# Kernel tuning notes

Hardware: AMD Instinct MI355X
Metric: run time of the kernel (lower is better)

## Reference

```python
import jax, jax.numpy as jnp
import numpy as np

LN_EPS = 1e-5


def setup_inputs() -> dict:
    N, E, D = 50000, 800000, 128
    H = 4 * D
    key = jax.random.key(0)
    ks = jax.random.split(key, 8)
    h = jax.random.normal(ks[0], (N, D), dtype=jnp.float32)
    e_ij = jax.random.normal(ks[1], (E, D), dtype=jnp.float32)
    src = jax.random.randint(ks[2], (E,), 0, N, dtype=jnp.int32)
    dst = jax.random.randint(ks[3], (E,), 0, N, dtype=jnp.int32)
    # MLP params (torch nn.Linear default-style scale)
    W1 = jax.random.normal(ks[4], (D, H), dtype=jnp.float32) / np.sqrt(D)
    b1 = jnp.zeros((H,), dtype=jnp.float32)
    W2 = jax.random.normal(ks[5], (H, D), dtype=jnp.float32) / np.sqrt(H)
    b2 = jnp.zeros((D,), dtype=jnp.float32)
    gamma = jnp.ones((D,), dtype=jnp.float32)
    beta = jnp.zeros((D,), dtype=jnp.float32)
    return {"h": h, "e_ij": e_ij, "src": src, "dst": dst,
            "W1": W1, "b1": b1, "W2": W2, "b2": b2,
            "gamma": gamma, "beta": beta}


def reference(h, e_ij, src, dst, W1, b1, W2, b2, gamma, beta):
    N = h.shape[0]
    # update_all(copy_u('h'), sum): sum source-node features at each destination
    neigh = jax.ops.segment_sum(h[src], dst, num_segments=N)
    # update_all(copy_edge('e_ij'), sum): sum edge features at each destination
    u_edge = jax.ops.segment_sum(e_ij, dst, num_segments=N)
    u = neigh + u_edge                      # [N, D]
    # MLP: D -> 4D -> D with ReLU, then residual
    hid = jax.nn.relu(u @ W1 + b1)          # [N, 4D]
    out = hid @ W2 + b2 + h                 # [N, D]
    # LayerNorm over feature dim
    mean = jnp.mean(out, axis=-1, keepdims=True)
    var = jnp.var(out, axis=-1, keepdims=True)
    normed = (out - mean) * jax.lax.rsqrt(var + LN_EPS)
    # dropout with training=False is identity
    return normed * gamma + beta
```

## Files before the change

kernel.cpp:

```cpp
#include <hip/hip_runtime.h>

#define BM 64

typedef __bf16 bf16x8 __attribute__((ext_vector_type(8)));
typedef float f32x4 __attribute__((ext_vector_type(4)));
typedef float f4 __attribute__((ext_vector_type(4)));

__device__ __forceinline__ unsigned short f2bf(float x) {
  unsigned int u = __builtin_bit_cast(unsigned int, x);
  u += 0x7fffu + ((u >> 16) & 1u);
  return (unsigned short)(u >> 16);
}

__device__ __forceinline__ int swz(int row, int col) {
  return (row * 128 + col) ^ ((row & 7) << 3);
}

__device__ __forceinline__ f4 ntload4(const float* p) {
  return __builtin_nontemporal_load((const f4*)p);
}

__device__ __forceinline__ int wave_incl_scan(int v, int lane) {
  #pragma unroll
  for (int off = 1; off < 64; off <<= 1) {
    int t = __shfl_up(v, off, 64);
    if (lane >= off) v += t;
  }
  return v;
}

__global__ __launch_bounds__(256) void prep_weights(
    const float* __restrict__ W1, const float* __restrict__ W2,
    unsigned short* __restrict__ W1T, unsigned short* __restrict__ W2T,
    int* __restrict__ counts, int N) {
  int t = blockIdx.x * 256 + threadIdx.x;
  if (t < N) counts[t] = 0;
  {
    int hh = t >> 7, kk = t & 127;
    W1T[t] = f2bf(W1[kk * 512 + hh]);
  }
  {
    int dd = t >> 9, hh = t & 511;
    W2T[t] = f2bf(W2[hh * 128 + dd]);
  }
}

__global__ __launch_bounds__(256) void hist_dst(const int* __restrict__ dst,
                                                int* counts, int E) {
  int i = blockIdx.x * 256 + threadIdx.x;
  if (i < E) atomicAdd(&counts[dst[i]], 1);
}

__global__ __launch_bounds__(256) void scan1(const int* __restrict__ counts,
                                             int* offs, int* btot, int N) {
  int i = blockIdx.x * 256 + threadIdx.x;
  int lane = threadIdx.x & 63, wv = threadIdx.x >> 6;
  int v = (i < N) ? counts[i] : 0;
  int incl = wave_incl_scan(v, lane);
  __shared__ int wt[4];
  if (lane == 63) wt[wv] = incl;
  __syncthreads();
  int wpre = 0;
  for (int w = 0; w < wv; ++w) wpre += wt[w];
  if (i < N) offs[i] = wpre + incl - v;
  if (threadIdx.x == 255) btot[blockIdx.x] = wpre + incl;
}

__global__ __launch_bounds__(64) void scan2(int* btot, int nb) {
  int lane = threadIdx.x;
  __shared__ int carry_s;
  if (lane == 0) carry_s = 0;
  __syncthreads();
  for (int base = 0; base < nb; base += 64) {
    int i = base + lane;
    int v = (i < nb) ? btot[i] : 0;
    int incl = wave_incl_scan(v, lane);
    int carry = carry_s;
    if (i < nb) btot[i] = carry + incl - v;
    __syncthreads();
    if (lane == 63) carry_s = carry + incl;
    __syncthreads();
  }
}

__global__ __launch_bounds__(256) void scan3(int* offs, const int* __restrict__ btot,
                                             int N) {
  int i = blockIdx.x * 256 + threadIdx.x;
  if (i < N) offs[i] += btot[blockIdx.x];
}

__global__ __launch_bounds__(256) void build_perm(const int* __restrict__ dst,
                                                  const int* __restrict__ src,
                                                  int* offs, int2* perm2, int E) {
  int i = blockIdx.x * 256 + threadIdx.x;
  if (i < E) {
    int p = atomicAdd(&offs[dst[i]], 1);
    perm2[p] = make_int2(i, src[i]);
  }
}

__global__ __launch_bounds__(256) void gather_sum(
    const float* __restrict__ hfeat, const float* __restrict__ eij,
    const int2* __restrict__ perm2,
    const int* __restrict__ offs, const int* __restrict__ counts,
    float* __restrict__ u, int N) {
  int node = blockIdx.x * 4 + (threadIdx.x >> 6);
  if (node >= N) return;
  int lane = threadIdx.x & 63;
  int half = lane >> 5, c4 = (lane & 31) * 4;
  int cnt = counts[node];
  int beg = offs[node] - cnt;
  f4 acc = (f4){0.f, 0.f, 0.f, 0.f};
  for (int base = 0; base < cnt; base += 64) {
    int m = cnt - base; if (m > 64) m = 64;
    int2 es = perm2[beg + base + (lane < m ? lane : m - 1)];
    int k = 0;
    for (; 2 * k + 8 <= m; k += 4) {
      int i0 = 2 * k + half;
      int e0 = __shfl(es.x, i0, 64),     s0 = __shfl(es.y, i0, 64);
      int e1 = __shfl(es.x, i0 + 2, 64), s1 = __shfl(es.y, i0 + 2, 64);
      int e2 = __shfl(es.x, i0 + 4, 64), s2 = __shfl(es.y, i0 + 4, 64);
      int e3 = __shfl(es.x, i0 + 6, 64), s3 = __shfl(es.y, i0 + 6, 64);
      f4 ev0 = ntload4(eij + (size_t)e0 * 128 + c4);
      f4 ev1 = ntload4(eij + (size_t)e1 * 128 + c4);
      f4 ev2 = ntload4(eij + (size_t)e2 * 128 + c4);
      f4 ev3 = ntload4(eij + (size_t)e3 * 128 + c4);
      f4 hv0 = *(const f4*)(hfeat + (size_t)s0 * 128 + c4);
      f4 hv1 = *(const f4*)(hfeat + (size_t)s1 * 128 + c4);
      f4 hv2 = *(const f4*)(hfeat + (size_t)s2 * 128 + c4);
      f4 hv3 = *(const f4*)(hfeat + (size_t)s3 * 128 + c4);
      acc += (ev0 + hv0) + (ev1 + hv1) + (ev2 + hv2) + (ev3 + hv3);
    }
    for (; 2 * k < m; ++k) {
      int idx = 2 * k + half;
      int e = __shfl(es.x, idx & 63, 64), s = __shfl(es.y, idx & 63, 64);
      if (idx < m) {
        f4 ev = ntload4(eij + (size_t)e * 128 + c4);
        f4 hv = *(const f4*)(hfeat + (size_t)s * 128 + c4);
        acc += ev + hv;
      }
    }
  }
  acc.x += __shfl_xor(acc.x, 32, 64);
  acc.y += __shfl_xor(acc.y, 32, 64);
  acc.z += __shfl_xor(acc.z, 32, 64);
  acc.w += __shfl_xor(acc.w, 32, 64);
  if (half == 0) *(f4*)(u + (size_t)node * 128 + c4) = acc;
}

__global__ __launch_bounds__(256, 2) void fused_mlp_ln(
    float* uo, const float* __restrict__ hfeat,
    const unsigned short* __restrict__ W1T, const unsigned short* __restrict__ W2T,
    const float* __restrict__ b1, const float* __restrict__ b2,
    const float* __restrict__ gma, const float* __restrict__ bta, int N) {
  __shared__ unsigned short As[BM * 128];
  __shared__ unsigned short Hs[BM * 128];
  __shared__ unsigned short Bs[128 * 128];

  const int tid = threadIdx.x;
  const int wave = tid >> 6, lane = tid & 63;
  const int lo = lane & 15, hi = lane >> 4;
  const int bm0 = blockIdx.x * BM;
  const int arow = wave * 16 + lo;

  #pragma unroll
  for (int i = 0; i < 8; ++i) {
    int q = i * 256 + tid;
    int r = q >> 5, c4 = (q & 31) * 4;
    f4 v = (f4){0.f, 0.f, 0.f, 0.f};
    if (bm0 + r < N) v = *(const f4*)(uo + (size_t)(bm0 + r) * 128 + c4);
    uint2 bv;
    bv.x = (unsigned)f2bf(v.x) | ((unsigned)f2bf(v.y) << 16);
    bv.y = (unsigned)f2bf(v.z) | ((unsigned)f2bf(v.w) << 16);
    *(uint2*)(&As[swz(r, c4)]) = bv;
  }

  f32x4 acc2[8];
  #pragma unroll
  for (int n = 0; n < 8; ++n) acc2[n] = (f32x4){0.f, 0.f, 0.f, 0.f};

  for (int c = 0; c < 4; ++c) {
    __syncthreads();
    #pragma unroll
    for (int i = 0; i < 8; ++i) {
      int q = i * 256 + tid;
      int r = q >> 4, c8 = (q & 15) * 8;
      uint4 w = *(const uint4*)(W1T + ((size_t)(c * 128 + r) * 128 + c8));
      *(uint4*)(&Bs[swz(r, c8)]) = w;
    }
    __syncthreads();

    f32x4 acc1[8];
    #pragma unroll
    for (int n = 0; n < 8; ++n) acc1[n] = (f32x4){0.f, 0.f, 0.f, 0.f};
    #pragma unroll
    for (int kk = 0; kk < 4; ++kk) {
      bf16x8 a = *(const bf16x8*)(&As[swz(arow, kk * 32 + hi * 8)]);
      #pragma unroll
      for (int n = 0; n < 8; ++n) {
        bf16x8 b = *(const bf16x8*)(&Bs[swz(n * 16 + lo, kk * 32 + hi * 8)]);
        acc1[n] = __builtin_amdgcn_mfma_f32_16x16x32_bf16(a, b, acc1[n], 0, 0, 0);
      }
    }
    #pragma unroll
    for (int n = 0; n < 8; ++n) {
      float bb = b1[c * 128 + n * 16 + lo];
      #pragma unroll
      for (int j = 0; j < 4; ++j) {
        float v = acc1[n][j] + bb;
        v = v > 0.f ? v : 0.f;
        Hs[swz(wave * 16 + hi * 4 + j, n * 16 + lo)] = f2bf(v);
      }
    }
    __syncthreads();
    #pragma unroll
    for (int i = 0; i < 8; ++i) {
      int q = i * 256 + tid;
      int r = q >> 4, c8 = (q & 15) * 8;
      uint4 w = *(const uint4*)(W2T + ((size_t)r * 512 + c * 128 + c8));
      *(uint4*)(&Bs[swz(r, c8)]) = w;
    }
    __syncthreads();
    #pragma unroll
    for (int kk = 0; kk < 4; ++kk) {
      bf16x8 a = *(const bf16x8*)(&Hs[swz(arow, kk * 32 + hi * 8)]);
      #pragma unroll
      for (int n = 0; n < 8; ++n) {
        bf16x8 b = *(const bf16x8*)(&Bs[swz(n * 16 + lo, kk * 32 + hi * 8)]);
        acc2[n] = __builtin_amdgcn_mfma_f32_16x16x32_bf16(a, b, acc2[n], 0, 0, 0);
      }
    }
  }

  float b2v[8], gv[8], bv2[8];
  #pragma unroll
  for (int n = 0; n < 8; ++n) {
    int d = n * 16 + lo;
    b2v[n] = b2[d]; gv[n] = gma[d]; bv2[n] = bta[d];
  }
  #pragma unroll
  for (int j = 0; j < 4; ++j) {
    int m = wave * 16 + hi * 4 + j;
    int grow = bm0 + m;
    bool valid = grow < N;
    float vals[8];
    float s = 0.f, s2 = 0.f;
    #pragma unroll
    for (int n = 0; n < 8; ++n) {
      float hres = valid ? hfeat[(size_t)grow * 128 + n * 16 + lo] : 0.f;
      float v = acc2[n][j] + b2v[n] + hres;
      vals[n] = v;
      s += v; s2 += v * v;
    }
    #pragma unroll
    for (int mk = 1; mk < 16; mk <<= 1) {
      s  += __shfl_xor(s, mk, 64);
      s2 += __shfl_xor(s2, mk, 64);
    }
    float mean = s * (1.f / 128.f);
    float var = s2 * (1.f / 128.f) - mean * mean;
    float inv = rsqrtf(var + 1e-5f);
    if (valid) {
      #pragma unroll
      for (int n = 0; n < 8; ++n) {
        uo[(size_t)grow * 128 + n * 16 + lo] = (vals[n] - mean) * inv * gv[n] + bv2[n];
      }
    }
  }
}

extern "C" void kernel_launch(void* const* d_in, const int* in_sizes, int n_in,
                              void* d_out, int out_size, void* d_ws, size_t ws_size,
                              hipStream_t stream) {
  (void)n_in; (void)out_size; (void)ws_size;
  const float* hfeat = (const float*)d_in[0];
  const float* eij   = (const float*)d_in[1];
  const int*   src   = (const int*)d_in[2];
  const int*   dst   = (const int*)d_in[3];
  const float* W1    = (const float*)d_in[4];
  const float* b1    = (const float*)d_in[5];
  const float* W2    = (const float*)d_in[6];
  const float* b2    = (const float*)d_in[7];
  const float* gma   = (const float*)d_in[8];
  const float* bta   = (const float*)d_in[9];
  float* out = (float*)d_out;

  int N = in_sizes[0] / 128;
  int E = in_sizes[2];
  int nb1 = (N + 255) / 256;

  char* ws = (char*)d_ws;
  unsigned short* W1T = (unsigned short*)ws;              ws += 512 * 128 * 2;
  unsigned short* W2T = (unsigned short*)ws;              ws += 128 * 512 * 2;
  int* counts = (int*)ws;                                 ws += (size_t)N * 4;
  int* offs   = (int*)ws;                                 ws += (size_t)N * 4;
  int* btot   = (int*)ws;                                 ws += ((nb1 + 63) / 64) * 64 * 4;
  ws = (char*)(((uintptr_t)ws + 255) & ~(uintptr_t)255);
  int2* perm2 = (int2*)ws;                                ws += (size_t)E * 8;

  prep_weights<<<256, 256, 0, stream>>>(W1, W2, W1T, W2T, counts, N);
  hist_dst<<<(E + 255) / 256, 256, 0, stream>>>(dst, counts, E);
  scan1<<<nb1, 256, 0, stream>>>(counts, offs, btot, N);
  scan2<<<1, 64, 0, stream>>>(btot, nb1);
  scan3<<<nb1, 256, 0, stream>>>(offs, btot, N);
  build_perm<<<(E + 255) / 256, 256, 0, stream>>>(dst, src, offs, perm2, E);

  gather_sum<<<(N + 3) / 4, 256, 0, stream>>>(hfeat, eij, perm2, offs, counts,
                                              out, N);

  fused_mlp_ln<<<(N + BM - 1) / BM, 256, 0, stream>>>(out, hfeat, W1T, W2T,
                                                      b1, b2, gma, bta, N);
}
```

Before: 264.5 us.

## Merge three scan kernels into one single-block scan and deepen gather unroll

Replaces the three-kernel multi-block prefix scan with one 1024-thread block in which each thread serially scans a contiguous chunk, removing two launches and the block-total buffer. Adds an 8-edge unrolled path in gather_sum so more independent loads are in flight, and adds a min-blocks launch bound to limit registers. The single-block scan uses only one CU and does strided, uncoalesced serial reads. The wider unroll raises register pressure.

```diff
diff --git a/kernel.cpp b/kernel.cpp
--- a/kernel.cpp
+++ b/kernel.cpp
@@ -51,42 +51,23 @@
   if (i < E) atomicAdd(&counts[dst[i]], 1);
 }
 
-__global__ __launch_bounds__(256) void scan1(const int* __restrict__ counts,
-                                             int* offs, int* btot, int N) {
-  int i = blockIdx.x * 256 + threadIdx.x;
-  int lane = threadIdx.x & 63, wv = threadIdx.x >> 6;
-  int v = (i < N) ? counts[i] : 0;
-  int incl = wave_incl_scan(v, lane);
-  __shared__ int wt[4];
-  if (lane == 63) wt[wv] = incl;
+__global__ __launch_bounds__(1024) void scan_all(const int* __restrict__ counts,
+                                                 int* __restrict__ offs, int N) {
+  __shared__ int wsum[16];
+  const int tid = threadIdx.x, lane = tid & 63, wv = tid >> 6;
+  const int per = (N + 1023) >> 10;
+  int b0 = tid * per, b1 = b0 + per;
+  if (b0 > N) b0 = N;
+  if (b1 > N) b1 = N;
+  int s = 0;
+  for (int i = b0; i < b1; ++i) s += counts[i];
+  int incl = wave_incl_scan(s, lane);
+  if (lane == 63) wsum[wv] = incl;
   __syncthreads();
   int wpre = 0;
-  for (int w = 0; w < wv; ++w) wpre += wt[w];
-  if (i < N) offs[i] = wpre + incl - v;
-  if (threadIdx.x == 255) btot[blockIdx.x] = wpre + incl;
-}
-
-__global__ __launch_bounds__(64) void scan2(int* btot, int nb) {
-  int lane = threadIdx.x;
-  __shared__ int carry_s;
-  if (lane == 0) carry_s = 0;
-  __syncthreads();
-  for (int base = 0; base < nb; base += 64) {
-    int i = base + lane;
-    int v = (i < nb) ? btot[i] : 0;
-    int incl = wave_incl_scan(v, lane);
-    int carry = carry_s;
-    if (i < nb) btot[i] = carry + incl - v;
-    __syncthreads();
-    if (lane == 63) carry_s = carry + incl;
-    __syncthreads();
-  }
-}
-
-__global__ __launch_bounds__(256) void scan3(int* offs, const int* __restrict__ btot,
-                                             int N) {
-  int i = blockIdx.x * 256 + threadIdx.x;
-  if (i < N) offs[i] += btot[blockIdx.x];
+  for (int w = 0; w < wv; ++w) wpre += wsum[w];
+  int excl = wpre + incl - s;
+  for (int i = b0; i < b1; ++i) { offs[i] = excl; excl += counts[i]; }
 }
 
 __global__ __launch_bounds__(256) void build_perm(const int* __restrict__ dst,
@@ -99,7 +80,7 @@
   }
 }
 
-__global__ __launch_bounds__(256) void gather_sum(
+__global__ __launch_bounds__(256, 4) void gather_sum(
     const float* __restrict__ hfeat, const float* __restrict__ eij,
     const int2* __restrict__ perm2,
     const int* __restrict__ offs, const int* __restrict__ counts,
@@ -115,6 +96,35 @@
     int m = cnt - base; if (m > 64) m = 64;
     int2 es = perm2[beg + base + (lane < m ? lane : m - 1)];
     int k = 0;
+    for (; 2 * k + 16 <= m; k += 8) {
+      int i0 = 2 * k + half;
+      int e0 = __shfl(es.x, i0, 64),      s0 = __shfl(es.y, i0, 64);
+      int e1 = __shfl(es.x, i0 + 2, 64),  s1 = __shfl(es.y, i0 + 2, 64);
+      int e2 = __shfl(es.x, i0 + 4, 64),  s2 = __shfl(es.y, i0 + 4, 64);
+      int e3 = __shfl(es.x, i0 + 6, 64),  s3 = __shfl(es.y, i0 + 6, 64);
+      int e4 = __shfl(es.x, i0 + 8, 64),  s4 = __shfl(es.y, i0 + 8, 64);
+      int e5 = __shfl(es.x, i0 + 10, 64), s5 = __shfl(es.y, i0 + 10, 64);
+      int e6 = __shfl(es.x, i0 + 12, 64), s6 = __shfl(es.y, i0 + 12, 64);
+      int e7 = __shfl(es.x, i0 + 14, 64), s7 = __shfl(es.y, i0 + 14, 64);
+      f4 ev0 = ntload4(eij + (size_t)e0 * 128 + c4);
+      f4 ev1 = ntload4(eij + (size_t)e1 * 128 + c4);
+      f4 ev2 = ntload4(eij + (size_t)e2 * 128 + c4);
+      f4 ev3 = ntload4(eij + (size_t)e3 * 128 + c4);
+      f4 ev4 = ntload4(eij + (size_t)e4 * 128 + c4);
+      f4 ev5 = ntload4(eij + (size_t)e5 * 128 + c4);
+      f4 ev6 = ntload4(eij + (size_t)e6 * 128 + c4);
+      f4 ev7 = ntload4(eij + (size_t)e7 * 128 + c4);
+      f4 hv0 = *(const f4*)(hfeat + (size_t)s0 * 128 + c4);
+      f4 hv1 = *(const f4*)(hfeat + (size_t)s1 * 128 + c4);
+      f4 hv2 = *(const f4*)(hfeat + (size_t)s2 * 128 + c4);
+      f4 hv3 = *(const f4*)(hfeat + (size_t)s3 * 128 + c4);
+      f4 hv4 = *(const f4*)(hfeat + (size_t)s4 * 128 + c4);
+      f4 hv5 = *(const f4*)(hfeat + (size_t)s5 * 128 + c4);
+      f4 hv6 = *(const f4*)(hfeat + (size_t)s6 * 128 + c4);
+      f4 hv7 = *(const f4*)(hfeat + (size_t)s7 * 128 + c4);
+      acc += (ev0 + hv0) + (ev1 + hv1) + (ev2 + hv2) + (ev3 + hv3)
+           + (ev4 + hv4) + (ev5 + hv5) + (ev6 + hv6) + (ev7 + hv7);
+    }
     for (; 2 * k + 8 <= m; k += 4) {
       int i0 = 2 * k + half;
       int e0 = __shfl(es.x, i0, 64),     s0 = __shfl(es.y, i0, 64);
@@ -287,22 +297,18 @@
 
   int N = in_sizes[0] / 128;
   int E = in_sizes[2];
-  int nb1 = (N + 255) / 256;
 
   char* ws = (char*)d_ws;
   unsigned short* W1T = (unsigned short*)ws;              ws += 512 * 128 * 2;
   unsigned short* W2T = (unsigned short*)ws;              ws += 128 * 512 * 2;
   int* counts = (int*)ws;                                 ws += (size_t)N * 4;
   int* offs   = (int*)ws;                                 ws += (size_t)N * 4;
-  int* btot   = (int*)ws;                                 ws += ((nb1 + 63) / 64) * 64 * 4;
   ws = (char*)(((uintptr_t)ws + 255) & ~(uintptr_t)255);
   int2* perm2 = (int2*)ws;                                ws += (size_t)E * 8;
 
   prep_weights<<<256, 256, 0, stream>>>(W1, W2, W1T, W2T, counts, N);
   hist_dst<<<(E + 255) / 256, 256, 0, stream>>>(dst, counts, E);
-  scan1<<<nb1, 256, 0, stream>>>(counts, offs, btot, N);
-  scan2<<<1, 64, 0, stream>>>(btot, nb1);
-  scan3<<<nb1, 256, 0, stream>>>(offs, btot, N);
+  scan_all<<<1, 1024, 0, stream>>>(counts, offs, N);
   build_perm<<<(E + 255) / 256, 256, 0, stream>>>(dst, src, offs, perm2, E);
 
   gather_sum<<<(N + 3) / 4, 256, 0, stream>>>(hfeat, eij, perm2, offs, counts,
```

Result: slower. 325.3 us (+23.0%).
